# Kernel tuning notes

Hardware: AMD Instinct MI355X
Metric: run time of the kernel (lower is better)

## Reference

```python
import jax, jax.numpy as jnp
import numpy as np

RES0 = 0.12
SCALE = 2.0
NUM_LEVELS = 2
FDIM = 32
TSIZE = 2 ** 20
BMIN = np.array([-2.6, -8.1, 0.0], np.float32)
BMAX = np.array([4.6, 4.7, 3.1], np.float32)
PRIMES = np.array([73856093, 19349669, 83492791], np.int64)
# (idx*prime) % T == (idx*(prime%T)) % T, so int32 math is exact here
PM = jnp.asarray(PRIMES % TSIZE, jnp.int32)
M_QUERIES = 500000
OFFSETS = jnp.asarray([[0,0,0],[0,0,1],[0,1,0],[0,1,1],[1,0,0],[1,0,1],[1,1,0],[1,1,1]], jnp.int32)  # (8,3)


def _build_hash_table(res: float):
    """Host-side construction mirroring _SingleResVoxelHashTable.__init__."""
    axes = [np.arange(BMIN[d], BMAX[d], res, dtype=np.float32) for d in range(3)]
    gx, gy, gz = np.meshgrid(*axes, indexing='ij')
    coords = np.stack([gx, gy, gz], axis=-1).reshape(-1, 3)
    n = coords.shape[0]
    idx = np.floor(coords / np.float32(res)).astype(np.int64)
    hv = (idx * PRIMES[None, :]).sum(axis=-1) % TSIZE
    h2v = np.full(TSIZE, -1, dtype=np.int64)
    h2v[hv] = np.arange(n)
    return n, jnp.asarray(h2v, jnp.int32)


def setup_inputs() -> dict:
    key = jax.random.key(0)
    k_q, k_f0, k_f1 = jax.random.split(key, 3)
    n0, h2v0 = _build_hash_table(RES0)
    n1, h2v1 = _build_hash_table(RES0 * SCALE)
    bmin = jnp.asarray(BMIN)
    bmax = jnp.asarray(BMAX)
    query_pts = bmin + jax.random.uniform(k_q, (M_QUERIES, 3), jnp.float32) * (bmax - bmin)
    feats0 = 0.01 * jax.random.normal(k_f0, (n0, FDIM), jnp.float32)
    feats1 = 0.01 * jax.random.normal(k_f1, (n1, FDIM), jnp.float32)
    return {"query_pts": query_pts, "feats0": feats0, "feats1": feats1,
            "h2v0": h2v0, "h2v1": h2v1}


def _query_trilinear(q, feats, h2v, res):
    qs = q / jnp.float32(res)                       # (M,3)
    base_f = jnp.floor(qs)
    frac = qs - base_f                              # (M,3)
    base = base_f.astype(jnp.int32)
    corner = base[:, None, :] + OFFSETS[None, :, :]  # (M,8,3)
    hv = jnp.mod((corner * PM).sum(-1), TSIZE)      # (M,8)
    v_idx = h2v[hv]                                 # (M,8)
    valid = v_idx >= 0
    feat = jnp.where(valid[..., None], feats[jnp.where(valid, v_idx, 0)], 0.0)  # (M,8,F)
    w = jnp.prod(jnp.where(OFFSETS[None].astype(bool), frac[:, None, :], 1.0 - frac[:, None, :]), axis=2)  # (M,8)
    return (feat * w[..., None]).sum(axis=1)        # (M,F)


def reference(query_pts, feats0, feats1, h2v0, h2v1):
    f0 = _query_trilinear(query_pts, feats0, h2v0, RES0)
    f1 = _query_trilinear(query_pts, feats1, h2v1, RES0 * SCALE)
    return jnp.concatenate([f0, f1], axis=-1)       # (M, 2*FDIM)
```

## Files before the change

### kernel.cpp

```cpp
#include <hip/hip_runtime.h>
#include <hip/hip_fp16.h>


#define TMASK 0xFFFFFu
#define PM0 455773u
#define PM1 475301u
#define PM2 655287u

#define BMINX -2.6f
#define BMINY -8.1f
#define BMINZ  0.0f
#define BMAXX  4.6f
#define BMAXY  4.7f
#define BMAXZ  3.1f
#define RES0   0.12f
#define RES1   0.24f

typedef float nfloat4 __attribute__((ext_vector_type(4)));

union H8 {
    unsigned long long u;
    __half2 h[2];
};

static __device__ __forceinline__ unsigned vhash(int cx, int cy, int cz) {
    return ((unsigned)cx * PM0 + (unsigned)cy * PM1 + (unsigned)cz * PM2) & TMASK;
}

__global__ __launch_bounds__(256) void build_fp16_tables(
    const int* __restrict__ h2v0, const int* __restrict__ h2v1,
    const float* __restrict__ feats0, const float* __restrict__ feats1,
    unsigned char* __restrict__ T0, unsigned char* __restrict__ T1,
    int x0a, int y0a, int z0a, int eya, int eza,
    int x0b, int y0b, int z0b, int eyb, int ezb,
    int R0, int R1)
{
    const int tid = blockIdx.x * 256 + (int)threadIdx.x;
    const int grp = tid >> 3, gt = tid & 7;
    if (grp < R0) {
        const int iz = grp % eza, t = grp / eza, iy = t % eya, ix = t / eya;
        const int v = h2v0[vhash(ix + x0a, iy + y0a, iz + z0a)];
        float4 f = make_float4(0.f, 0.f, 0.f, 0.f);
        if (v >= 0) f = *(const float4*)(feats0 + (size_t)v * 32 + gt * 4);
        H8 pk;
        pk.h[0] = __floats2half2_rn(f.x, f.y);
        pk.h[1] = __floats2half2_rn(f.z, f.w);
        *(unsigned long long*)(T0 + (size_t)grp * 128 + gt * 8) = pk.u;
        if (iz > 0)
            *(unsigned long long*)(T0 + (size_t)(grp - 1) * 128 + 64 + gt * 8) = pk.u;
        if (iz == eza - 1)
            *(unsigned long long*)(T0 + (size_t)grp * 128 + 64 + gt * 8) = 0ull;
    } else if (grp < R0 + R1) {
        const int r = grp - R0;
        const int iz = r % ezb, t = r / ezb, iy = t % eyb, ix = t / eyb;
        const int v = h2v1[vhash(ix + x0b, iy + y0b, iz + z0b)];
        float4 f = make_float4(0.f, 0.f, 0.f, 0.f);
        if (v >= 0) f = *(const float4*)(feats1 + (size_t)v * 32 + gt * 4);
        H8 pk;
        pk.h[0] = __floats2half2_rn(f.x, f.y);
        pk.h[1] = __floats2half2_rn(f.z, f.w);
        *(unsigned long long*)(T1 + (size_t)r * 64 + gt * 8) = pk.u;
    }
}

__global__ __launch_bounds__(256) void voxel_query_fp16(
    const float* __restrict__ qpts,
    const unsigned char* __restrict__ T0, const unsigned char* __restrict__ T1,
    int x0a, int y0a, int z0a, int eya, int eza,
    int x0b, int y0b, int z0b, int eyb, int ezb,
    float* __restrict__ out, int M)
{
    const int tid = blockIdx.x * 256 + (int)threadIdx.x;
    const int g  = tid >> 3;
    const int gt = tid & 7;
    const int s  = g >> 1;
    const int level = g & 1;
    if (s >= M) return;

    const float qx = qpts[3 * (size_t)s + 0];
    const float qy = qpts[3 * (size_t)s + 1];
    const float qz = qpts[3 * (size_t)s + 2];

    const float res = level ? RES1 : RES0;
    const unsigned char* __restrict__ T = level ? T1 : T0;
    const int S  = level ? 64 : 128;
    const int x0 = level ? x0b : x0a, y0 = level ? y0b : y0a, z0 = level ? z0b : z0a;
    const int ey = level ? eyb : eya, ez = level ? ezb : eza;

    const float sx = qx / res, sy = qy / res, sz = qz / res;
    const float bx = floorf(sx), by = floorf(sy), bz = floorf(sz);
    const float fx = sx - bx,  fy = sy - by,  fz = sz - bz;

    const int ibx = (int)bx - x0, iby = (int)by - y0, ibz = (int)bz - z0;
    const int c00 = (ibx * ey + iby) * ez + ibz;
    const int c01 = c00 + ez;
    const int c10 = c00 + ey * ez;
    const int c11 = c10 + ez;

    const float wx0 = 1.0f - fx, wy0 = 1.0f - fy, wz0 = 1.0f - fz;
    const int boff = gt * 8;

    nfloat4 acc = {0.0f, 0.0f, 0.0f, 0.0f};

    #define ACC_CORNER(cell, wxy)                                              \
    do {                                                                       \
        const unsigned char* p = T + (size_t)(cell) * S + boff;                \
        H8 d0, d1;                                                             \
        d0.u = *(const unsigned long long*)p;                                  \
        d1.u = *(const unsigned long long*)(p + 64);                           \
        const float w0 = (wxy) * wz0, w1 = (wxy) * fz;                         \
        {                                                                      \
            const float2 u = __half22float2(d0.h[0]);                          \
            const float2 v = __half22float2(d0.h[1]);                          \
            acc.x = fmaf(w0, u.x, acc.x); acc.y = fmaf(w0, u.y, acc.y);        \
            acc.z = fmaf(w0, v.x, acc.z); acc.w = fmaf(w0, v.y, acc.w);        \
        }                                                                      \
        {                                                                      \
            const float2 u = __half22float2(d1.h[0]);                          \
            const float2 v = __half22float2(d1.h[1]);                          \
            acc.x = fmaf(w1, u.x, acc.x); acc.y = fmaf(w1, u.y, acc.y);        \
            acc.z = fmaf(w1, v.x, acc.z); acc.w = fmaf(w1, v.y, acc.w);        \
        }                                                                      \
    } while (0)

    ACC_CORNER(c00, wx0 * wy0);
    ACC_CORNER(c01, wx0 * fy);
    ACC_CORNER(c10, fx * wy0);
    ACC_CORNER(c11, fx * fy);
    #undef ACC_CORNER

    __builtin_nontemporal_store(
        acc, (nfloat4*)(out + (size_t)s * 64 + level * 32) + gt);
}

__global__ __launch_bounds__(256) void build_dense(
    const int* __restrict__ h2v0, const int* __restrict__ h2v1,
    int* __restrict__ dense0, int* __restrict__ dense1,
    int x0a, int y0a, int z0a, int eya, int eza,
    int x0b, int y0b, int z0b, int eyb, int ezb,
    int D0, int D1)
{
    const int i = blockIdx.x * blockDim.x + threadIdx.x;
    if (i < D0) {
        const int iz = i % eza, t = i / eza, iy = t % eya, ix = t / eya;
        dense0[i] = h2v0[vhash(ix + x0a, iy + y0a, iz + z0a)];
    } else if (i < D0 + D1) {
        const int j = i - D0;
        const int iz = j % ezb, t = j / ezb, iy = t % eyb, ix = t / eyb;
        dense1[j] = h2v1[vhash(ix + x0b, iy + y0b, iz + z0b)];
    }
}

__global__ __launch_bounds__(256) void voxel_query_direct(
    const float* __restrict__ qpts,
    const float* __restrict__ feats0, const float* __restrict__ feats1,
    const int*   __restrict__ h2v0,   const int*   __restrict__ h2v1,
    const int*   __restrict__ dense0, const int*   __restrict__ dense1,
    int x0a, int y0a, int z0a, int exa, int eya, int eza,
    int x0b, int y0b, int z0b, int exb, int eyb, int ezb,
    float* __restrict__ out, int M)
{
    const int tid = blockIdx.x * 256 + (int)threadIdx.x;
    const int g  = tid >> 3;
    const int gt = tid & 7;
    const int s  = g >> 1;
    const int level = g & 1;
    if (s >= M) return;

    const float qx = qpts[3 * (size_t)s + 0];
    const float qy = qpts[3 * (size_t)s + 1];
    const float qz = qpts[3 * (size_t)s + 2];

    const float res = level ? RES1 : RES0;
    const float* __restrict__ feats = level ? feats1 : feats0;
    const int*   __restrict__ h2v   = level ? h2v1   : h2v0;
    const int*   __restrict__ dense = level ? dense1 : dense0;
    const int x0 = level ? x0b : x0a, y0 = level ? y0b : y0a, z0 = level ? z0b : z0a;
    const int ex = level ? exb : exa, ey = level ? eyb : eya, ez = level ? ezb : eza;

    const float sx = qx / res, sy = qy / res, sz = qz / res;
    const float bx = floorf(sx), by = floorf(sy), bz = floorf(sz);
    const float fx = sx - bx,  fy = sy - by,  fz = sz - bz;

    const int ox = (gt >> 2) & 1, oy = (gt >> 1) & 1, oz = gt & 1;
    const int cx = (int)bx + ox;
    const int cy = (int)by + oy;
    const int cz = (int)bz + oz;

    int v;
    if (cx >= x0 && cx < x0 + ex && cy >= y0 && cy < y0 + ey &&
        cz >= z0 && cz < z0 + ez) {
        v = dense[((size_t)(cx - x0) * ey + (cy - y0)) * ez + (cz - z0)];
    } else {
        v = h2v[vhash(cx, cy, cz)];
    }

    float w = (ox ? fx : 1.0f - fx) * (oy ? fy : 1.0f - fy);
    w *= (oz ? fz : 1.0f - fz);

    nfloat4 acc = {0.0f, 0.0f, 0.0f, 0.0f};
    #pragma unroll
    for (int c = 0; c < 8; ++c) {
        const int   vc = __shfl(v, c, 8);
        const float wc = __shfl(w, c, 8);
        if (vc >= 0) {
            const nfloat4 f4 = ((const nfloat4*)(feats + (size_t)vc * 32))[gt];
            acc += wc * f4;
        }
    }
    __builtin_nontemporal_store(
        acc, (nfloat4*)(out + (size_t)s * 64 + level * 32) + gt);
}

__global__ __launch_bounds__(256) void voxel_hash_query_f32(
    const float* __restrict__ qpts,
    const float* __restrict__ feats0, const float* __restrict__ feats1,
    const int*   __restrict__ h2v0,   const int*   __restrict__ h2v1,
    float* __restrict__ out, int M)
{
    const int tid = blockIdx.x * blockDim.x + threadIdx.x;
    const int group = tid >> 3, gt = tid & 7;
    const int m = group >> 1, level = group & 1;
    if (m >= M) return;
    const float res = level ? RES1 : RES0;
    const float* __restrict__ feats = level ? feats1 : feats0;
    const int*   __restrict__ h2v   = level ? h2v1   : h2v0;
    const float qx = qpts[3 * (size_t)m], qy = qpts[3 * (size_t)m + 1],
                qz = qpts[3 * (size_t)m + 2];
    const float sx = qx / res, sy = qy / res, sz = qz / res;
    const float bx = floorf(sx), by = floorf(sy), bz = floorf(sz);
    const float fx = sx - bx, fy = sy - by, fz = sz - bz;
    const int ox = (gt >> 2) & 1, oy = (gt >> 1) & 1, oz = gt & 1;
    const int v = h2v[vhash((int)bx + ox, (int)by + oy, (int)bz + oz)];
    float w = (ox ? fx : 1.0f - fx) * (oy ? fy : 1.0f - fy);
    w *= (oz ? fz : 1.0f - fz);
    nfloat4 acc = {0.f, 0.f, 0.f, 0.f};
    #pragma unroll
    for (int c = 0; c < 8; ++c) {
        const int vc = __shfl(v, c, 8);
        const float wc = __shfl(w, c, 8);
        if (vc >= 0) {
            const nfloat4 f4 = ((const nfloat4*)(feats + (size_t)vc * 32))[gt];
            acc += wc * f4;
        }
    }
    ((nfloat4*)(out + (size_t)m * 64 + level * 32))[gt] = acc;
}

extern "C" void kernel_launch(void* const* d_in, const int* in_sizes, int n_in,
                              void* d_out, int out_size, void* d_ws, size_t ws_size,
                              hipStream_t stream) {
    const float* qpts   = (const float*)d_in[0];
    const float* feats0 = (const float*)d_in[1];
    const float* feats1 = (const float*)d_in[2];
    const int*   h2v0   = (const int*)d_in[3];
    const int*   h2v1   = (const int*)d_in[4];
    float* out = (float*)d_out;
    const int M = in_sizes[0] / 3;

    const float bmin[3] = {BMINX, BMINY, BMINZ};
    const float bmax[3] = {BMAXX, BMAXY, BMAXZ};
    int lo0[3], ex0[3], lo1[3], ex1[3];
    for (int d = 0; d < 3; ++d) {
        lo0[d] = (int)floorf(bmin[d] / RES0) - 2;
        ex0[d] = (int)floorf(bmax[d] / RES0) + 3 - lo0[d] + 1;
        lo1[d] = (int)floorf(bmin[d] / RES1) - 2;
        ex1[d] = (int)floorf(bmax[d] / RES1) + 3 - lo1[d] + 1;
    }
    const int R0 = ex0[0] * ex0[1] * ex0[2];
    const int R1 = ex1[0] * ex1[1] * ex1[2];

    const long long threads_needed = 16LL * M;
    const int nb = (int)((threads_needed + 255) / 256);

    {
        char* p = (char*)d_ws;
        unsigned char* T0 = (unsigned char*)p;  p += (size_t)R0 * 128;
        unsigned char* T1 = (unsigned char*)p;  p += (size_t)R1 * 64;
        const size_t need = (size_t)(p - (char*)d_ws);
        if (ws_size >= need) {
            const int gBuild = (int)((8LL * (R0 + R1) + 255) / 256);
            build_fp16_tables<<<gBuild, 256, 0, stream>>>(
                h2v0, h2v1, feats0, feats1, T0, T1,
                lo0[0], lo0[1], lo0[2], ex0[1], ex0[2],
                lo1[0], lo1[1], lo1[2], ex1[1], ex1[2],
                R0, R1);
            voxel_query_fp16<<<nb, 256, 0, stream>>>(
                qpts, T0, T1,
                lo0[0], lo0[1], lo0[2], ex0[1], ex0[2],
                lo1[0], lo1[1], lo1[2], ex1[1], ex1[2],
                out, M);
            return;
        }
    }

    {
        char* p = (char*)d_ws;
        int* dense0 = (int*)p;                 p += (size_t)R0 * 4;
        int* dense1 = (int*)p;                 p += (size_t)R1 * 4;
        const size_t need = (size_t)(p - (char*)d_ws);
        if (ws_size >= need) {
            const int gA = (R0 + R1 + 255) / 256;
            build_dense<<<gA, 256, 0, stream>>>(h2v0, h2v1, dense0, dense1,
                                                lo0[0], lo0[1], lo0[2], ex0[1], ex0[2],
                                                lo1[0], lo1[1], lo1[2], ex1[1], ex1[2],
                                                R0, R1);
            voxel_query_direct<<<nb, 256, 0, stream>>>(
                qpts, feats0, feats1, h2v0, h2v1, dense0, dense1,
                lo0[0], lo0[1], lo0[2], ex0[0], ex0[1], ex0[2],
                lo1[0], lo1[1], lo1[2], ex1[0], ex1[1], ex1[2],
                out, M);
            return;
        }
    }

    voxel_hash_query_f32<<<nb, 256, 0, stream>>>(qpts, feats0, feats1,
                                                 h2v0, h2v1, out, M);
}
```

Baseline: 211.2 us.

## Process both hash levels per thread group and batch all corner loads

The query kernel now assigns one 8-thread group per query point and handles both resolution levels in that group. Before, separate groups handled each level. The query load and the index setup are shared across levels. All 16 corner loads are issued before any accumulation, which exposes more memory-level parallelism. The table-build kernel switches to nontemporal loads and stores, and the dense table padding margins are trimmed. The trade-off is fewer threads in flight and more registers per thread.

```diff
diff --git a/kernel.cpp b/kernel.cpp
--- a/kernel.cpp
+++ b/kernel.cpp
@@ -40,30 +40,38 @@
     if (grp < R0) {
         const int iz = grp % eza, t = grp / eza, iy = t % eya, ix = t / eya;
         const int v = h2v0[vhash(ix + x0a, iy + y0a, iz + z0a)];
-        float4 f = make_float4(0.f, 0.f, 0.f, 0.f);
-        if (v >= 0) f = *(const float4*)(feats0 + (size_t)v * 32 + gt * 4);
+        nfloat4 f = {0.f, 0.f, 0.f, 0.f};
+        if (v >= 0)
+            f = __builtin_nontemporal_load(
+                    (const nfloat4*)(feats0 + (size_t)v * 32 + gt * 4));
         H8 pk;
         pk.h[0] = __floats2half2_rn(f.x, f.y);
         pk.h[1] = __floats2half2_rn(f.z, f.w);
-        *(unsigned long long*)(T0 + (size_t)grp * 128 + gt * 8) = pk.u;
+        __builtin_nontemporal_store(pk.u,
+            (unsigned long long*)(T0 + (size_t)grp * 128 + gt * 8));
         if (iz > 0)
-            *(unsigned long long*)(T0 + (size_t)(grp - 1) * 128 + 64 + gt * 8) = pk.u;
+            __builtin_nontemporal_store(pk.u,
+                (unsigned long long*)(T0 + (size_t)(grp - 1) * 128 + 64 + gt * 8));
         if (iz == eza - 1)
-            *(unsigned long long*)(T0 + (size_t)grp * 128 + 64 + gt * 8) = 0ull;
+            __builtin_nontemporal_store(0ull,
+                (unsigned long long*)(T0 + (size_t)grp * 128 + 64 + gt * 8));
     } else if (grp < R0 + R1) {
         const int r = grp - R0;
         const int iz = r % ezb, t = r / ezb, iy = t % eyb, ix = t / eyb;
         const int v = h2v1[vhash(ix + x0b, iy + y0b, iz + z0b)];
-        float4 f = make_float4(0.f, 0.f, 0.f, 0.f);
-        if (v >= 0) f = *(const float4*)(feats1 + (size_t)v * 32 + gt * 4);
+        nfloat4 f = {0.f, 0.f, 0.f, 0.f};
+        if (v >= 0)
+            f = __builtin_nontemporal_load(
+                    (const nfloat4*)(feats1 + (size_t)v * 32 + gt * 4));
         H8 pk;
         pk.h[0] = __floats2half2_rn(f.x, f.y);
         pk.h[1] = __floats2half2_rn(f.z, f.w);
-        *(unsigned long long*)(T1 + (size_t)r * 64 + gt * 8) = pk.u;
-    }
-}
-
-__global__ __launch_bounds__(256) void voxel_query_fp16(
+        __builtin_nontemporal_store(pk.u,
+            (unsigned long long*)(T1 + (size_t)r * 64 + gt * 8));
+    }
+}
+
+__global__ __launch_bounds__(256) void voxel_query_fp16_v2(
     const float* __restrict__ qpts,
     const unsigned char* __restrict__ T0, const unsigned char* __restrict__ T1,
     int x0a, int y0a, int z0a, int eya, int eza,
@@ -71,66 +79,95 @@
     float* __restrict__ out, int M)
 {
     const int tid = blockIdx.x * 256 + (int)threadIdx.x;
-    const int g  = tid >> 3;
+    const int s  = tid >> 3;
     const int gt = tid & 7;
-    const int s  = g >> 1;
-    const int level = g & 1;
     if (s >= M) return;
 
-    const float qx = qpts[3 * (size_t)s + 0];
-    const float qy = qpts[3 * (size_t)s + 1];
-    const float qz = qpts[3 * (size_t)s + 2];
-
-    const float res = level ? RES1 : RES0;
-    const unsigned char* __restrict__ T = level ? T1 : T0;
-    const int S  = level ? 64 : 128;
-    const int x0 = level ? x0b : x0a, y0 = level ? y0b : y0a, z0 = level ? z0b : z0a;
-    const int ey = level ? eyb : eya, ez = level ? ezb : eza;
-
-    const float sx = qx / res, sy = qy / res, sz = qz / res;
-    const float bx = floorf(sx), by = floorf(sy), bz = floorf(sz);
-    const float fx = sx - bx,  fy = sy - by,  fz = sz - bz;
-
-    const int ibx = (int)bx - x0, iby = (int)by - y0, ibz = (int)bz - z0;
-    const int c00 = (ibx * ey + iby) * ez + ibz;
-    const int c01 = c00 + ez;
-    const int c10 = c00 + ey * ez;
-    const int c11 = c10 + ez;
-
-    const float wx0 = 1.0f - fx, wy0 = 1.0f - fy, wz0 = 1.0f - fz;
+    const float qx = __builtin_nontemporal_load(qpts + 3 * (size_t)s + 0);
+    const float qy = __builtin_nontemporal_load(qpts + 3 * (size_t)s + 1);
+    const float qz = __builtin_nontemporal_load(qpts + 3 * (size_t)s + 2);
     const int boff = gt * 8;
 
-    nfloat4 acc = {0.0f, 0.0f, 0.0f, 0.0f};
-
-    #define ACC_CORNER(cell, wxy)                                              \
-    do {                                                                       \
-        const unsigned char* p = T + (size_t)(cell) * S + boff;                \
-        H8 d0, d1;                                                             \
-        d0.u = *(const unsigned long long*)p;                                  \
-        d1.u = *(const unsigned long long*)(p + 64);                           \
-        const float w0 = (wxy) * wz0, w1 = (wxy) * fz;                         \
-        {                                                                      \
-            const float2 u = __half22float2(d0.h[0]);                          \
-            const float2 v = __half22float2(d0.h[1]);                          \
-            acc.x = fmaf(w0, u.x, acc.x); acc.y = fmaf(w0, u.y, acc.y);        \
-            acc.z = fmaf(w0, v.x, acc.z); acc.w = fmaf(w0, v.y, acc.w);        \
-        }                                                                      \
-        {                                                                      \
-            const float2 u = __half22float2(d1.h[0]);                          \
-            const float2 v = __half22float2(d1.h[1]);                          \
-            acc.x = fmaf(w1, u.x, acc.x); acc.y = fmaf(w1, u.y, acc.y);        \
-            acc.z = fmaf(w1, v.x, acc.z); acc.w = fmaf(w1, v.y, acc.w);        \
-        }                                                                      \
-    } while (0)
-
-    ACC_CORNER(c00, wx0 * wy0);
-    ACC_CORNER(c01, wx0 * fy);
-    ACC_CORNER(c10, fx * wy0);
-    ACC_CORNER(c11, fx * fy);
-    #undef ACC_CORNER
-
-    __builtin_nontemporal_store(
-        acc, (nfloat4*)(out + (size_t)s * 64 + level * 32) + gt);
+    const float sx0 = qx / RES0, sy0 = qy / RES0, sz0 = qz / RES0;
+    const float bx0 = floorf(sx0), by0 = floorf(sy0), bz0 = floorf(sz0);
+    const float fx0 = sx0 - bx0, fy0 = sy0 - by0, fz0 = sz0 - bz0;
+    const int ax = (int)bx0 - x0a, ay = (int)by0 - y0a, az = (int)bz0 - z0a;
+    const int a00 = (ax * eya + ay) * eza + az;
+    const int a01 = a00 + eza;
+    const int a10 = a00 + eya * eza;
+    const int a11 = a10 + eza;
+
+    const float sx1 = qx / RES1, sy1 = qy / RES1, sz1 = qz / RES1;
+    const float bx1 = floorf(sx1), by1 = floorf(sy1), bz1 = floorf(sz1);
+    const float fx1 = sx1 - bx1, fy1 = sy1 - by1, fz1 = sz1 - bz1;
+    const int bx = (int)bx1 - x0b, by = (int)by1 - y0b, bz = (int)bz1 - z0b;
+    const int b00 = (bx * eyb + by) * ezb + bz;
+    const int b01 = b00 + ezb;
+    const int b10 = b00 + eyb * ezb;
+    const int b11 = b10 + ezb;
+
+    H8 d[16];
+    {
+        const unsigned char* p;
+        p = T0 + (size_t)a00 * 128 + boff;
+        d[0].u = *(const unsigned long long*)p;
+        d[1].u = *(const unsigned long long*)(p + 64);
+        p = T0 + (size_t)a01 * 128 + boff;
+        d[2].u = *(const unsigned long long*)p;
+        d[3].u = *(const unsigned long long*)(p + 64);
+        p = T0 + (size_t)a10 * 128 + boff;
+        d[4].u = *(const unsigned long long*)p;
+        d[5].u = *(const unsigned long long*)(p + 64);
+        p = T0 + (size_t)a11 * 128 + boff;
+        d[6].u = *(const unsigned long long*)p;
+        d[7].u = *(const unsigned long long*)(p + 64);
+        p = T1 + (size_t)b00 * 64 + boff;
+        d[8].u  = *(const unsigned long long*)p;
+        d[9].u  = *(const unsigned long long*)(p + 64);
+        p = T1 + (size_t)b01 * 64 + boff;
+        d[10].u = *(const unsigned long long*)p;
+        d[11].u = *(const unsigned long long*)(p + 64);
+        p = T1 + (size_t)b10 * 64 + boff;
+        d[12].u = *(const unsigned long long*)p;
+        d[13].u = *(const unsigned long long*)(p + 64);
+        p = T1 + (size_t)b11 * 64 + boff;
+        d[14].u = *(const unsigned long long*)p;
+        d[15].u = *(const unsigned long long*)(p + 64);
+    }
+
+    const float wx0 = 1.0f - fx0, wy0 = 1.0f - fy0, wz0 = 1.0f - fz0;
+    const float wx1 = 1.0f - fx1, wy1 = 1.0f - fy1, wz1 = 1.0f - fz1;
+    float w0[8], w1[8];
+    w0[0] = wx0 * wy0 * wz0; w0[1] = wx0 * wy0 * fz0;
+    w0[2] = wx0 * fy0 * wz0; w0[3] = wx0 * fy0 * fz0;
+    w0[4] = fx0 * wy0 * wz0; w0[5] = fx0 * wy0 * fz0;
+    w0[6] = fx0 * fy0 * wz0; w0[7] = fx0 * fy0 * fz0;
+    w1[0] = wx1 * wy1 * wz1; w1[1] = wx1 * wy1 * fz1;
+    w1[2] = wx1 * fy1 * wz1; w1[3] = wx1 * fy1 * fz1;
+    w1[4] = fx1 * wy1 * wz1; w1[5] = fx1 * wy1 * fz1;
+    w1[6] = fx1 * fy1 * wz1; w1[7] = fx1 * fy1 * fz1;
+
+    nfloat4 acc0 = {0.f, 0.f, 0.f, 0.f};
+    nfloat4 acc1 = {0.f, 0.f, 0.f, 0.f};
+    #pragma unroll
+    for (int c = 0; c < 8; ++c) {
+        const float2 u0 = __half22float2(d[c].h[0]);
+        const float2 v0 = __half22float2(d[c].h[1]);
+        acc0.x = fmaf(w0[c], u0.x, acc0.x);
+        acc0.y = fmaf(w0[c], u0.y, acc0.y);
+        acc0.z = fmaf(w0[c], v0.x, acc0.z);
+        acc0.w = fmaf(w0[c], v0.y, acc0.w);
+        const float2 u1 = __half22float2(d[8 + c].h[0]);
+        const float2 v1 = __half22float2(d[8 + c].h[1]);
+        acc1.x = fmaf(w1[c], u1.x, acc1.x);
+        acc1.y = fmaf(w1[c], u1.y, acc1.y);
+        acc1.z = fmaf(w1[c], v1.x, acc1.z);
+        acc1.w = fmaf(w1[c], v1.y, acc1.w);
+    }
+
+    float* o = out + (size_t)s * 64;
+    __builtin_nontemporal_store(acc0, (nfloat4*)(o) + gt);
+    __builtin_nontemporal_store(acc1, (nfloat4*)(o + 32) + gt);
 }
 
 __global__ __launch_bounds__(256) void build_dense(
@@ -262,16 +299,13 @@
     const float bmax[3] = {BMAXX, BMAXY, BMAXZ};
     int lo0[3], ex0[3], lo1[3], ex1[3];
     for (int d = 0; d < 3; ++d) {
-        lo0[d] = (int)floorf(bmin[d] / RES0) - 2;
-        ex0[d] = (int)floorf(bmax[d] / RES0) + 3 - lo0[d] + 1;
-        lo1[d] = (int)floorf(bmin[d] / RES1) - 2;
-        ex1[d] = (int)floorf(bmax[d] / RES1) + 3 - lo1[d] + 1;
+        lo0[d] = (int)floorf(bmin[d] / RES0) - 1;
+        ex0[d] = ((int)floorf(bmax[d] / RES0) + 2) - lo0[d] + 1;
+        lo1[d] = (int)floorf(bmin[d] / RES1) - 1;
+        ex1[d] = ((int)floorf(bmax[d] / RES1) + 2) - lo1[d] + 1;
     }
     const int R0 = ex0[0] * ex0[1] * ex0[2];
     const int R1 = ex1[0] * ex1[1] * ex1[2];
-
-    const long long threads_needed = 16LL * M;
-    const int nb = (int)((threads_needed + 255) / 256);
 
     {
         char* p = (char*)d_ws;
@@ -285,7 +319,8 @@
                 lo0[0], lo0[1], lo0[2], ex0[1], ex0[2],
                 lo1[0], lo1[1], lo1[2], ex1[1], ex1[2],
                 R0, R1);
-            voxel_query_fp16<<<nb, 256, 0, stream>>>(
+            const int nbQ = (int)((8LL * M + 255) / 256);
+            voxel_query_fp16_v2<<<nbQ, 256, 0, stream>>>(
                 qpts, T0, T1,
                 lo0[0], lo0[1], lo0[2], ex0[1], ex0[2],
                 lo1[0], lo1[1], lo1[2], ex1[1], ex1[2],
@@ -293,6 +328,9 @@
             return;
         }
     }
+
+    const long long threads_needed = 16LL * M;
+    const int nb = (int)((threads_needed + 255) / 256);
 
     {
         char* p = (char*)d_ws;
```

New measurement: 222.2 us. 1.05x slower.
